# Performance work log

Measured on AMD Instinct MI355X. Metric: run time of the kernel, lower is better.

The kernel has to match this reference:

```python
import jax, jax.numpy as jnp
import numpy as np

N_HEADS = 16
D_MODEL = 1024
TOTAL = 8192
N_SEQ = 8
SEQ_LEN = TOTAL // N_SEQ


def setup_inputs() -> dict:
    key = jax.random.key(0)
    ks = jax.random.split(key, 12)
    f = jnp.float32
    d = D_MODEL
    inp = {
        "query": jax.random.normal(ks[0], (TOTAL, d), f),
        "key": jax.random.normal(ks[1], (TOTAL, d), f),
        "value": jax.random.normal(ks[2], (TOTAL, d), f),
        "seq_lengths_q": jnp.full((N_SEQ,), SEQ_LEN, jnp.int64 if jax.config.jax_enable_x64 else jnp.int32),
        "seq_lengths_kv": jnp.full((N_SEQ,), SEQ_LEN, jnp.int64 if jax.config.jax_enable_x64 else jnp.int32),
        "Wq": jax.random.normal(ks[3], (d, d), f) * 0.02,
        "bq": jnp.zeros((d,), f),
        "Wk": jax.random.normal(ks[4], (d, d), f) * 0.02,
        "bk": jnp.zeros((d,), f),
        "Wv": jax.random.normal(ks[5], (d, d), f) * 0.02,
        "bv": jnp.zeros((d,), f),
        "Wo": jax.random.normal(ks[6], (d, d), f) * 0.02,
        "bo": jnpp if False else jnp.zeros((d,), f),
    }
    return inp


def reference(query, key, value, seq_lengths_q, seq_lengths_kv, Wq, bq, Wk, bk, Wv, bv, Wo, bo):
    Tq, d = query.shape
    Tkv = key.shape[0]
    H = N_HEADS
    Dh = d // H
    B = seq_lengths_q.shape[0]
    Lq = Tq // B  # equal-length packed sequences
    Lkv = Tkv // B
    scale = 1.0 / jnp.sqrt(jnp.asarray(Dh, query.dtype))

    # torch Linear: x @ W.T + b
    Q = (query @ Wq.T + bq).reshape(H, Tq, Dh)   # NOTE: raw view, no transpose
    K = (key @ Wk.T + bk).reshape(H, Tkv, Dh)    # (replicates original's view semantics)
    V = (value @ Wv.T + bv).reshape(H, Tkv, Dh)

    # Block-diagonal mask over equal-length sequences == per-block attention.
    Qb = Q.reshape(H, B, Lq, Dh)
    Kb = K.reshape(H, B, Lkv, Dh)
    Vb = V.reshape(H, B, Lkv, Dh)

    scores = jnp.einsum("hbqd,hbkd->hbqk", Qb, Kb) * scale  # [H,B,Lq,Lkv]
    probs = jax.nn.softmax(scores, axis=-1)
    attn = jnp.einsum("hbqk,hbkd->hbqd", probs, Vb)          # [H,B,Lq,Dh]

    attn = attn.reshape(H, Tq, Dh).reshape(Tq, d)  # matches .view(total_q, d_model)
    out = attn @ Wo.T + bo
    return out
```

## Files before the change

kernel.cpp:

```cpp
#include <hip/hip_runtime.h>
#include <hip/hip_bf16.h>

#define TOTAL   8192
#define DMODEL  1024
#define NHEADS  16
#define NSEQ    8
#define DH      64

typedef float  f32x4 __attribute__((ext_vector_type(4)));
typedef short  s16x8 __attribute__((ext_vector_type(8)));
typedef unsigned short u16;
typedef u16    u16x8 __attribute__((ext_vector_type(8)));

__device__ __forceinline__ u16 f2bf_rne(float x) {
  union { float f; unsigned u; } v; v.f = x;
  unsigned r = v.u + 0x7FFFu + ((v.u >> 16) & 1u);
  return (u16)(r >> 16);
}

__device__ __forceinline__ void async_cp16(const u16* g, u16* l) {
  __builtin_amdgcn_global_load_lds(
      (const __attribute__((address_space(1))) unsigned int*)g,
      (__attribute__((address_space(3))) unsigned int*)l, 16, 0, 0);
}

__global__ __launch_bounds__(256) void cvt8(const float* __restrict__ src,
                                            u16* __restrict__ dst) {
  long i = ((long)blockIdx.x * 256 + threadIdx.x) * 8;
  float4 a = *reinterpret_cast<const float4*>(src + i);
  float4 b = *reinterpret_cast<const float4*>(src + i + 4);
  u16x8 o;
  o[0] = f2bf_rne(a.x); o[1] = f2bf_rne(a.y); o[2] = f2bf_rne(a.z); o[3] = f2bf_rne(a.w);
  o[4] = f2bf_rne(b.x); o[5] = f2bf_rne(b.y); o[6] = f2bf_rne(b.z); o[7] = f2bf_rne(b.w);
  *reinterpret_cast<u16x8*>(dst + i) = o;
}

template<bool OUT_BF16>
__global__ __launch_bounds__(256) void gemm_nt_async(const u16* __restrict__ A,
                                                     const u16* __restrict__ B,
                                                     const float* __restrict__ bias,
                                                     void* __restrict__ Cp) {
  __shared__ u16 As[128 * 32];
  __shared__ u16 Bs[128 * 32];
  const int tid  = threadIdx.x;
  const int lane = tid & 63;
  const int wv   = tid >> 6;
  const int quad = lane >> 4;
  const int m16  = lane & 15;
  const int wm   = (wv & 1) * 64;
  const int wn   = (wv >> 1) * 64;
  const long bm0 = (long)blockIdx.x * 128;
  const long bn0 = (long)blockIdx.y * 128;

  const int srow = lane >> 2;
  const int sk8  = (lane & 3) * 8;

  f32x4 acc[4][4] = {};

  const u16* Abase = A + bm0 * DMODEL;
  const u16* Bbase = B + bn0 * DMODEL;

  for (int k0 = 0; k0 < DMODEL; k0 += 32) {
    #pragma unroll
    for (int j = 0; j < 2; j++) {
      const int r   = j * 4 + wv;
      const int row = r * 16 + srow;
      async_cp16(Abase + (long)row * DMODEL + k0 + sk8, &As[r * 512]);
      async_cp16(Bbase + (long)row * DMODEL + k0 + sk8, &Bs[r * 512]);
    }
    __syncthreads();

    s16x8 af[4], bfr[4];
    #pragma unroll
    for (int i = 0; i < 4; i++)
      af[i] = *(const s16x8*)&As[(wm + i * 16 + m16) * 32 + quad * 8];
    #pragma unroll
    for (int j = 0; j < 4; j++)
      bfr[j] = *(const s16x8*)&Bs[(wn + j * 16 + m16) * 32 + quad * 8];
    #pragma unroll
    for (int i = 0; i < 4; i++)
      #pragma unroll
      for (int j = 0; j < 4; j++)
        acc[i][j] = __builtin_amdgcn_mfma_f32_16x16x32_bf16(af[i], bfr[j], acc[i][j], 0, 0, 0);
    __syncthreads();
  }

  #pragma unroll
  for (int j = 0; j < 4; j++) {
    const long col = bn0 + wn + j * 16 + m16;
    const float bj = bias[col];
    #pragma unroll
    for (int i = 0; i < 4; i++) {
      const long row0 = bm0 + wm + i * 16 + quad * 4;
      #pragma unroll
      for (int r = 0; r < 4; r++) {
        float v = acc[i][j][r] + bj;
        if constexpr (OUT_BF16)
          ((u16*)Cp)[(row0 + r) * DMODEL + col] = f2bf_rne(v);
        else
          ((float*)Cp)[(row0 + r) * DMODEL + col] = v;
      }
    }
  }
}

__global__ __launch_bounds__(256) void transpose_v(const u16* __restrict__ Vbf,
                                                   u16* __restrict__ Vt) {
  constexpr int TP = 72;
  __shared__ u16 tile[64 * TP];
  const int tid = threadIdx.x;
  const long base = (long)blockIdx.y * 65536;
  const int kt = blockIdx.x;
  {
    int k = tid >> 2, dh0 = (tid & 3) * 16;
    const u16* g = Vbf + base + (long)(kt * 64 + k) * 64 + dh0;
    u16x8 a = ((const u16x8*)g)[0];
    u16x8 b = ((const u16x8*)g)[1];
    #pragma unroll
    for (int i = 0; i < 8; i++) tile[(dh0 + i) * TP + k] = a[i];
    #pragma unroll
    for (int i = 0; i < 8; i++) tile[(dh0 + 8 + i) * TP + k] = b[i];
  }
  __syncthreads();
  {
    int dh = tid >> 2, k0 = (tid & 3) * 16;
    u16x8 a = *(const u16x8*)&tile[dh * TP + k0];
    u16x8 b = *(const u16x8*)&tile[dh * TP + k0 + 8];
    u16* g = Vt + base + (long)dh * 1024 + kt * 64 + k0;
    ((u16x8*)g)[0] = a;
    ((u16x8*)g)[1] = b;
  }
}

__global__ __launch_bounds__(256) void attn_kernel(const u16* __restrict__ Qbf,
                                                   const u16* __restrict__ Kbf,
                                                   const u16* __restrict__ Vt,
                                                   u16* __restrict__ Obf) {
  constexpr int KP = 72;
  constexpr int EP = 76;
  __shared__ u16 Ks[64 * KP];
  __shared__ u16 Vs[64 * KP];
  __shared__ u16 Es[4 * 16 * EP];
  const int tid  = threadIdx.x;
  const int lane = tid & 63;
  const int wv   = tid >> 6;
  const int quad = lane >> 4;
  const int m16  = lane & 15;
  const int qt   = blockIdx.y;
  const long base = (long)blockIdx.x * 65536;

  const int qrow = qt * 64 + wv * 16;
  s16x8 aq[2];
  #pragma unroll
  for (int s = 0; s < 2; s++)
    aq[s] = *(const s16x8*)(Qbf + base + (long)(qrow + m16) * 64 + s * 32 + quad * 8);

  f32x4 acc_o[4];
  f32x4 acc_d = {0.f, 0.f, 0.f, 0.f};
  #pragma unroll
  for (int n = 0; n < 4; n++) acc_o[n] = acc_d;

  union { u16x8 u; s16x8 s; } onesu;
  u16 ov = (m16 == 0) ? (u16)0x3F80 : (u16)0;
  #pragma unroll
  for (int i = 0; i < 8; i++) onesu.u[i] = ov;
  const s16x8 bones = onesu.s;

  const float SC = 0.125f * 1.44269504088896340736f;
  const int sr = tid >> 2;
  const int sk = (tid & 3) * 16;

  for (int nt = 0; nt < 16; nt++) {
    {
      const u16* g = Kbf + base + nt * 4096 + (long)sr * 64 + sk;
      u16x8 a = ((const u16x8*)g)[0];
      u16x8 b = ((const u16x8*)g)[1];
      *(u16x8*)&Ks[sr * KP + sk]     = a;
      *(u16x8*)&Ks[sr * KP + sk + 8] = b;
    }
    {
      const u16* g = Vt + base + (long)sr * 1024 + nt * 64 + sk;
      u16x8 a = ((const u16x8*)g)[0];
      u16x8 b = ((const u16x8*)g)[1];
      *(u16x8*)&Vs[sr * KP + sk]     = a;
      *(u16x8*)&Vs[sr * KP + sk + 8] = b;
    }
    __syncthreads();

    #pragma unroll
    for (int n = 0; n < 4; n++) {
      s16x8 bk0 = *(const s16x8*)&Ks[(n * 16 + m16) * KP + quad * 8];
      s16x8 bk1 = *(const s16x8*)&Ks[(n * 16 + m16) * KP + 32 + quad * 8];
      f32x4 s = {0.f, 0.f, 0.f, 0.f};
      s = __builtin_amdgcn_mfma_f32_16x16x32_bf16(aq[0], bk0, s, 0, 0, 0);
      s = __builtin_amdgcn_mfma_f32_16x16x32_bf16(aq[1], bk1, s, 0, 0, 0);
      #pragma unroll
      for (int r = 0; r < 4; r++) {
        float e = __builtin_amdgcn_exp2f(s[r] * SC);
        Es[(wv * 16 + quad * 4 + r) * EP + n * 16 + m16] = f2bf_rne(e);
      }
    }
    s16x8 ae0 = *(const s16x8*)&Es[(wv * 16 + m16) * EP + quad * 8];
    s16x8 ae1 = *(const s16x8*)&Es[(wv * 16 + m16) * EP + 32 + quad * 8];
    #pragma unroll
    for (int n = 0; n < 4; n++) {
      s16x8 bv0 = *(const s16x8*)&Vs[(n * 16 + m16) * KP + quad * 8];
      s16x8 bv1 = *(const s16x8*)&Vs[(n * 16 + m16) * KP + 32 + quad * 8];
      acc_o[n] = __builtin_amdgcn_mfma_f32_16x16x32_bf16(ae0, bv0, acc_o[n], 0, 0, 0);
      acc_o[n] = __builtin_amdgcn_mfma_f32_16x16x32_bf16(ae1, bv1, acc_o[n], 0, 0, 0);
    }
    acc_d = __builtin_amdgcn_mfma_f32_16x16x32_bf16(ae0, bones, acc_d, 0, 0, 0);
    acc_d = __builtin_amdgcn_mfma_f32_16x16x32_bf16(ae1, bones, acc_d, 0, 0, 0);
    __syncthreads();
  }

  #pragma unroll
  for (int r = 0; r < 4; r++) {
    float d = __shfl(acc_d[r], lane & 48);
    float rinv = 1.0f / d;
    const long orow = base + (long)(qrow + quad * 4 + r) * 64;
    #pragma unroll
    for (int n = 0; n < 4; n++)
      Obf[orow + n * 16 + m16] = f2bf_rne(acc_o[n][r] * rinv);
  }
}

extern "C" void kernel_launch(void* const* d_in, const int* in_sizes, int n_in,
                              void* d_out, int out_size, void* d_ws, size_t ws_size,
                              hipStream_t stream) {
  const float* query = (const float*)d_in[0];
  const float* key_  = (const float*)d_in[1];
  const float* value = (const float*)d_in[2];
  const float* Wq = (const float*)d_in[5];
  const float* bq = (const float*)d_in[6];
  const float* Wk = (const float*)d_in[7];
  const float* bk = (const float*)d_in[8];
  const float* Wv = (const float*)d_in[9];
  const float* bv = (const float*)d_in[10];
  const float* Wo = (const float*)d_in[11];
  const float* bo = (const float*)d_in[12];

  char* ws = (char*)d_ws;
  u16* Wbf = (u16*)(ws);
  u16* Xbf = (u16*)(ws + (8l << 20));
  u16* Qbf = (u16*)(ws + (24l << 20));
  u16* Kbf = (u16*)(ws + (40l << 20));
  u16* Vbf = (u16*)(ws + (56l << 20));
  u16* Vt  = Xbf;
  u16* Obf = Vbf;

  cvt8<<<512, 256, 0, stream>>>(Wq, Wbf + 0 * 1048576);
  cvt8<<<512, 256, 0, stream>>>(Wk, Wbf + 1 * 1048576);
  cvt8<<<512, 256, 0, stream>>>(Wv, Wbf + 2 * 1048576);
  cvt8<<<512, 256, 0, stream>>>(Wo, Wbf + 3 * 1048576);

  cvt8<<<4096, 256, 0, stream>>>(query, Xbf);
  gemm_nt_async<true><<<dim3(64, 8), 256, 0, stream>>>(Xbf, Wbf + 0 * 1048576, bq, Qbf);
  cvt8<<<4096, 256, 0, stream>>>(key_, Xbf);
  gemm_nt_async<true><<<dim3(64, 8), 256, 0, stream>>>(Xbf, Wbf + 1 * 1048576, bk, Kbf);
  cvt8<<<4096, 256, 0, stream>>>(value, Xbf);
  gemm_nt_async<true><<<dim3(64, 8), 256, 0, stream>>>(Xbf, Wbf + 2 * 1048576, bv, Vbf);

  transpose_v<<<dim3(16, 128), 256, 0, stream>>>(Vbf, Vt);

  attn_kernel<<<dim3(128, 16), 256, 0, stream>>>(Qbf, Kbf, Vt, Obf);

  gemm_nt_async<false><<<dim3(64, 8), 256, 0, stream>>>(Obf, Wbf + 3 * 1048576, bo, (float*)d_out);
}
```

Baseline: 356.0 us.

## Batch QKV projections into one launch and double query rows per attention block

Merges the four weight conversions into one launch. When the workspace is large enough, it also merges the three input conversions and the three QKV GEMMs into single batched launches using a z-grid. The attention kernel now processes 128 query rows per block (32 per wave), so each K/V tile loaded into shared memory is reused across twice as many queries, and the grid shrinks accordingly. This cuts launch overhead and per-row K/V traffic, at the cost of more registers and shared memory per block and a fallback path that depends on workspace size.

```diff
diff --git a/kernel.cpp b/kernel.cpp
--- a/kernel.cpp
+++ b/kernel.cpp
@@ -24,15 +24,103 @@
       (__attribute__((address_space(3))) unsigned int*)l, 16, 0, 0);
 }
 
-__global__ __launch_bounds__(256) void cvt8(const float* __restrict__ src,
-                                            u16* __restrict__ dst) {
-  long i = ((long)blockIdx.x * 256 + threadIdx.x) * 8;
+__device__ __forceinline__ void cvt8_one(const float* __restrict__ src,
+                                         u16* __restrict__ dst, long i) {
   float4 a = *reinterpret_cast<const float4*>(src + i);
   float4 b = *reinterpret_cast<const float4*>(src + i + 4);
   u16x8 o;
   o[0] = f2bf_rne(a.x); o[1] = f2bf_rne(a.y); o[2] = f2bf_rne(a.z); o[3] = f2bf_rne(a.w);
   o[4] = f2bf_rne(b.x); o[5] = f2bf_rne(b.y); o[6] = f2bf_rne(b.z); o[7] = f2bf_rne(b.w);
   *reinterpret_cast<u16x8*>(dst + i) = o;
+}
+
+__global__ __launch_bounds__(256) void cvt8(const float* __restrict__ src,
+                                            u16* __restrict__ dst) {
+  cvt8_one(src, dst, ((long)blockIdx.x * 256 + threadIdx.x) * 8);
+}
+
+__global__ __launch_bounds__(256) void cvt8_w4(const float* __restrict__ w0,
+                                               const float* __restrict__ w1,
+                                               const float* __restrict__ w2,
+                                               const float* __restrict__ w3,
+                                               u16* __restrict__ dst) {
+  const float* srcs[4] = {w0, w1, w2, w3};
+  cvt8_one(srcs[blockIdx.y], dst + (long)blockIdx.y * (DMODEL * (long)DMODEL),
+           ((long)blockIdx.x * 256 + threadIdx.x) * 8);
+}
+
+__global__ __launch_bounds__(256) void cvt8_x3(const float* __restrict__ x0,
+                                               const float* __restrict__ x1,
+                                               const float* __restrict__ x2,
+                                               u16* __restrict__ dst) {
+  const float* srcs[3] = {x0, x1, x2};
+  cvt8_one(srcs[blockIdx.y], dst + (long)blockIdx.y * (TOTAL * (long)DMODEL),
+           ((long)blockIdx.x * 256 + threadIdx.x) * 8);
+}
+
+template<bool OUT_BF16>
+__device__ __forceinline__ void gemm_core(const u16* __restrict__ A,
+                                          const u16* __restrict__ B,
+                                          const float* __restrict__ bias,
+                                          void* __restrict__ Cp,
+                                          long bm0, long bn0,
+                                          u16* As, u16* Bs) {
+  const int tid  = threadIdx.x;
+  const int lane = tid & 63;
+  const int wv   = tid >> 6;
+  const int quad = lane >> 4;
+  const int m16  = lane & 15;
+  const int wm   = (wv & 1) * 64;
+  const int wn   = (wv >> 1) * 64;
+  const int srow = lane >> 2;
+  const int sk8  = (lane & 3) * 8;
+
+  f32x4 acc[4][4] = {};
+  const u16* Abase = A + bm0 * DMODEL;
+  const u16* Bbase = B + bn0 * DMODEL;
+
+  for (int k0 = 0; k0 < DMODEL; k0 += 32) {
+    #pragma unroll
+    for (int j = 0; j < 2; j++) {
+      const int r   = j * 4 + wv;
+      const int row = r * 16 + srow;
+      async_cp16(Abase + (long)row * DMODEL + k0 + sk8, &As[r * 512]);
+      async_cp16(Bbase + (long)row * DMODEL + k0 + sk8, &Bs[r * 512]);
+    }
+    __syncthreads();
+
+    s16x8 af[4], bfr[4];
+    #pragma unroll
+    for (int i = 0; i < 4; i++)
+      af[i] = *(const s16x8*)&As[(wm + i * 16 + m16) * 32 + quad * 8];
+    #pragma unroll
+    for (int j = 0; j < 4; j++)
+      bfr[j] = *(const s16x8*)&Bs[(wn + j * 16 + m16) * 32 + quad * 8];
+    #pragma unroll
+    for (int i = 0; i < 4; i++)
+      #pragma unroll
+      for (int j = 0; j < 4; j++)
+        acc[i][j] = __builtin_amdgcn_mfma_f32_16x16x32_bf16(af[i], bfr[j], acc[i][j], 0, 0, 0);
+    __syncthreads();
+  }
+
+  #pragma unroll
+  for (int j = 0; j < 4; j++) {
+    const long col = bn0 + wn + j * 16 + m16;
+    const float bj = bias[col];
+    #pragma unroll
+    for (int i = 0; i < 4; i++) {
+      const long row0 = bm0 + wm + i * 16 + quad * 4;
+      #pragma unroll
+      for (int r = 0; r < 4; r++) {
+        float v = acc[i][j][r] + bj;
+        if constexpr (OUT_BF16)
+          ((u16*)Cp)[(row0 + r) * DMODEL + col] = f2bf_rne(v);
+        else
+          ((float*)Cp)[(row0 + r) * DMODEL + col] = v;
+      }
+    }
+  }
 }
 
 template<bool OUT_BF16>
@@ -42,66 +130,25 @@
                                                      void* __restrict__ Cp) {
   __shared__ u16 As[128 * 32];
   __shared__ u16 Bs[128 * 32];
-  const int tid  = threadIdx.x;
-  const int lane = tid & 63;
-  const int wv   = tid >> 6;
-  const int quad = lane >> 4;
-  const int m16  = lane & 15;
-  const int wm   = (wv & 1) * 64;
-  const int wn   = (wv >> 1) * 64;
-  const long bm0 = (long)blockIdx.x * 128;
-  const long bn0 = (long)blockIdx.y * 128;
-
-  const int srow = lane >> 2;
-  const int sk8  = (lane & 3) * 8;
-
-  f32x4 acc[4][4] = {};
-
-  const u16* Abase = A + bm0 * DMODEL;
-  const u16* Bbase = B + bn0 * DMODEL;
-
-  for (int k0 = 0; k0 < DMODEL; k0 += 32) {
-    #pragma unroll
-    for (int j = 0; j < 2; j++) {
-      const int r   = j * 4 + wv;
-      const int row = r * 16 + srow;
-      async_cp16(Abase + (long)row * DMODEL + k0 + sk8, &As[r * 512]);
-      async_cp16(Bbase + (long)row * DMODEL + k0 + sk8, &Bs[r * 512]);
-    }
-    __syncthreads();
-
-    s16x8 af[4], bfr[4];
-    #pragma unroll
-    for (int i = 0; i < 4; i++)
-      af[i] = *(const s16x8*)&As[(wm + i * 16 + m16) * 32 + quad * 8];
-    #pragma unroll
-    for (int j = 0; j < 4; j++)
-      bfr[j] = *(const s16x8*)&Bs[(wn + j * 16 + m16) * 32 + quad * 8];
-    #pragma unroll
-    for (int i = 0; i < 4; i++)
-      #pragma unroll
-      for (int j = 0; j < 4; j++)
-        acc[i][j] = __builtin_amdgcn_mfma_f32_16x16x32_bf16(af[i], bfr[j], acc[i][j], 0, 0, 0);
-    __syncthreads();
-  }
-
-  #pragma unroll
-  for (int j = 0; j < 4; j++) {
-    const long col = bn0 + wn + j * 16 + m16;
-    const float bj = bias[col];
-    #pragma unroll
-    for (int i = 0; i < 4; i++) {
-      const long row0 = bm0 + wm + i * 16 + quad * 4;
-      #pragma unroll
-      for (int r = 0; r < 4; r++) {
-        float v = acc[i][j][r] + bj;
-        if constexpr (OUT_BF16)
-          ((u16*)Cp)[(row0 + r) * DMODEL + col] = f2bf_rne(v);
-        else
-          ((float*)Cp)[(row0 + r) * DMODEL + col] = v;
-      }
-    }
-  }
+  gemm_core<OUT_BF16>(A, B, bias, Cp,
+                      (long)blockIdx.x * 128, (long)blockIdx.y * 128, As, Bs);
+}
+
+__global__ __launch_bounds__(256) void gemm_qkv(const u16* __restrict__ X3,
+                                                const u16* __restrict__ W3,
+                                                const float* __restrict__ bq,
+                                                const float* __restrict__ bk,
+                                                const float* __restrict__ bv,
+                                                u16* __restrict__ QKV) {
+  __shared__ u16 As[128 * 32];
+  __shared__ u16 Bs[128 * 32];
+  const int z = blockIdx.z;
+  const float* bias = (z == 0) ? bq : (z == 1) ? bk : bv;
+  gemm_core<true>(X3 + (long)z * (TOTAL * (long)DMODEL),
+                  W3 + (long)z * (DMODEL * (long)DMODEL),
+                  bias,
+                  QKV + (long)z * (TOTAL * (long)DMODEL),
+                  (long)blockIdx.x * 128, (long)blockIdx.y * 128, As, Bs);
 }
 
 __global__ __launch_bounds__(256) void transpose_v(const u16* __restrict__ Vbf,
@@ -137,10 +184,9 @@
                                                    const u16* __restrict__ Vt,
                                                    u16* __restrict__ Obf) {
   constexpr int KP = 72;
-  constexpr int EP = 76;
   __shared__ u16 Ks[64 * KP];
   __shared__ u16 Vs[64 * KP];
-  __shared__ u16 Es[4 * 16 * EP];
+  __shared__ u16 Es[4 * 32 * KP];
   const int tid  = threadIdx.x;
   const int lane = tid & 63;
   const int wv   = tid >> 6;
@@ -149,16 +195,16 @@
   const int qt   = blockIdx.y;
   const long base = (long)blockIdx.x * 65536;
 
-  const int qrow = qt * 64 + wv * 16;
-  s16x8 aq[2];
+  const int qrow0 = qt * 128 + wv * 32;
+  s16x8 aq[2][2];
   #pragma unroll
-  for (int s = 0; s < 2; s++)
-    aq[s] = *(const s16x8*)(Qbf + base + (long)(qrow + m16) * 64 + s * 32 + quad * 8);
-
-  f32x4 acc_o[4];
-  f32x4 acc_d = {0.f, 0.f, 0.f, 0.f};
-  #pragma unroll
-  for (int n = 0; n < 4; n++) acc_o[n] = acc_d;
+  for (int g = 0; g < 2; g++)
+    #pragma unroll
+    for (int s = 0; s < 2; s++)
+      aq[g][s] = *(const s16x8*)(Qbf + base + (long)(qrow0 + g * 16 + m16) * 64 + s * 32 + quad * 8);
+
+  f32x4 acc_o[2][4] = {};
+  f32x4 acc_d[2] = {};
 
   union { u16x8 u; s16x8 s; } onesu;
   u16 ov = (m16 == 0) ? (u16)0x3F80 : (u16)0;
@@ -191,38 +237,53 @@
     for (int n = 0; n < 4; n++) {
       s16x8 bk0 = *(const s16x8*)&Ks[(n * 16 + m16) * KP + quad * 8];
       s16x8 bk1 = *(const s16x8*)&Ks[(n * 16 + m16) * KP + 32 + quad * 8];
-      f32x4 s = {0.f, 0.f, 0.f, 0.f};
-      s = __builtin_amdgcn_mfma_f32_16x16x32_bf16(aq[0], bk0, s, 0, 0, 0);
-      s = __builtin_amdgcn_mfma_f32_16x16x32_bf16(aq[1], bk1, s, 0, 0, 0);
-      #pragma unroll
-      for (int r = 0; r < 4; r++) {
-        float e = __builtin_amdgcn_exp2f(s[r] * SC);
-        Es[(wv * 16 + quad * 4 + r) * EP + n * 16 + m16] = f2bf_rne(e);
+      #pragma unroll
+      for (int g = 0; g < 2; g++) {
+        f32x4 s = {0.f, 0.f, 0.f, 0.f};
+        s = __builtin_amdgcn_mfma_f32_16x16x32_bf16(aq[g][0], bk0, s, 0, 0, 0);
+        s = __builtin_amdgcn_mfma_f32_16x16x32_bf16(aq[g][1], bk1, s, 0, 0, 0);
+        #pragma unroll
+        for (int r = 0; r < 4; r++) {
+          float e = __builtin_amdgcn_exp2f(s[r] * SC);
+          Es[(wv * 32 + g * 16 + quad * 4 + r) * KP + n * 16 + m16] = f2bf_rne(e);
+        }
       }
     }
-    s16x8 ae0 = *(const s16x8*)&Es[(wv * 16 + m16) * EP + quad * 8];
-    s16x8 ae1 = *(const s16x8*)&Es[(wv * 16 + m16) * EP + 32 + quad * 8];
+    s16x8 ae[2][2];
+    #pragma unroll
+    for (int g = 0; g < 2; g++) {
+      ae[g][0] = *(const s16x8*)&Es[(wv * 32 + g * 16 + m16) * KP + quad * 8];
+      ae[g][1] = *(const s16x8*)&Es[(wv * 32 + g * 16 + m16) * KP + 32 + quad * 8];
+    }
     #pragma unroll
     for (int n = 0; n < 4; n++) {
       s16x8 bv0 = *(const s16x8*)&Vs[(n * 16 + m16) * KP + quad * 8];
       s16x8 bv1 = *(const s16x8*)&Vs[(n * 16 + m16) * KP + 32 + quad * 8];
-      acc_o[n] = __builtin_amdgcn_mfma_f32_16x16x32_bf16(ae0, bv0, acc_o[n], 0, 0, 0);
-      acc_o[n] = __builtin_amdgcn_mfma_f32_16x16x32_bf16(ae1, bv1, acc_o[n], 0, 0, 0);
-    }
-    acc_d = __builtin_amdgcn_mfma_f32_16x16x32_bf16(ae0, bones, acc_d, 0, 0, 0);
-    acc_d = __builtin_amdgcn_mfma_f32_16x16x32_bf16(ae1, bones, acc_d, 0, 0, 0);
+      #pragma unroll
+      for (int g = 0; g < 2; g++) {
+        acc_o[g][n] = __builtin_amdgcn_mfma_f32_16x16x32_bf16(ae[g][0], bv0, acc_o[g][n], 0, 0, 0);
+        acc_o[g][n] = __builtin_amdgcn_mfma_f32_16x16x32_bf16(ae[g][1], bv1, acc_o[g][n], 0, 0, 0);
+      }
+    }
+    #pragma unroll
+    for (int g = 0; g < 2; g++) {
+      acc_d[g] = __builtin_amdgcn_mfma_f32_16x16x32_bf16(ae[g][0], bones, acc_d[g], 0, 0, 0);
+      acc_d[g] = __builtin_amdgcn_mfma_f32_16x16x32_bf16(ae[g][1], bones, acc_d[g], 0, 0, 0);
+    }
     __syncthreads();
   }
 
   #pragma unroll
-  for (int r = 0; r < 4; r++) {
-    float d = __shfl(acc_d[r], lane & 48);
-    float rinv = 1.0f / d;
-    const long orow = base + (long)(qrow + quad * 4 + r) * 64;
-    #pragma unroll
-    for (int n = 0; n < 4; n++)
-      Obf[orow + n * 16 + m16] = f2bf_rne(acc_o[n][r] * rinv);
-  }
+  for (int g = 0; g < 2; g++)
+    #pragma unroll
+    for (int r = 0; r < 4; r++) {
+      float d = __shfl(acc_d[g][r], lane & 48);
+      float rinv = 1.0f / d;
+      const long orow = base + (long)(qrow0 + g * 16 + quad * 4 + r) * 64;
+      #pragma unroll
+      for (int n = 0; n < 4; n++)
+        Obf[orow + n * 16 + m16] = f2bf_rne(acc_o[g][n][r] * rinv);
+    }
 }
 
 extern "C" void kernel_launch(void* const* d_in, const int* in_sizes, int n_in,
@@ -241,29 +302,42 @@
   const float* bo = (const float*)d_in[12];
 
   char* ws = (char*)d_ws;
-  u16* Wbf = (u16*)(ws);
-  u16* Xbf = (u16*)(ws + (8l << 20));
-  u16* Qbf = (u16*)(ws + (24l << 20));
-  u16* Kbf = (u16*)(ws + (40l << 20));
-  u16* Vbf = (u16*)(ws + (56l << 20));
-  u16* Vt  = Xbf;
-  u16* Obf = Vbf;
-
-  cvt8<<<512, 256, 0, stream>>>(Wq, Wbf + 0 * 1048576);
-  cvt8<<<512, 256, 0, stream>>>(Wk, Wbf + 1 * 1048576);
-  cvt8<<<512, 256, 0, stream>>>(Wv, Wbf + 2 * 1048576);
-  cvt8<<<512, 256, 0, stream>>>(Wo, Wbf + 3 * 1048576);
-
-  cvt8<<<4096, 256, 0, stream>>>(query, Xbf);
-  gemm_nt_async<true><<<dim3(64, 8), 256, 0, stream>>>(Xbf, Wbf + 0 * 1048576, bq, Qbf);
-  cvt8<<<4096, 256, 0, stream>>>(key_, Xbf);
-  gemm_nt_async<true><<<dim3(64, 8), 256, 0, stream>>>(Xbf, Wbf + 1 * 1048576, bk, Kbf);
-  cvt8<<<4096, 256, 0, stream>>>(value, Xbf);
-  gemm_nt_async<true><<<dim3(64, 8), 256, 0, stream>>>(Xbf, Wbf + 2 * 1048576, bv, Vbf);
-
-  transpose_v<<<dim3(16, 128), 256, 0, stream>>>(Vbf, Vt);
-
-  attn_kernel<<<dim3(128, 16), 256, 0, stream>>>(Qbf, Kbf, Vt, Obf);
-
-  gemm_nt_async<false><<<dim3(64, 8), 256, 0, stream>>>(Obf, Wbf + 3 * 1048576, bo, (float*)d_out);
-}
+  const size_t FUSED_NEED = 104ull << 20;
+
+  if (ws_size >= FUSED_NEED) {
+    u16* Wbf = (u16*)(ws);
+    u16* QKV = (u16*)(ws + (8l << 20));
+    u16* Qbf = QKV;
+    u16* Kbf = QKV + 1 * (TOTAL * (long)DMODEL);
+    u16* Vbf = QKV + 2 * (TOTAL * (long)DMODEL);
+    u16* X3  = (u16*)(ws + (56l << 20));
+    u16* Vt  = X3;
+    u16* Obf = Vbf;
+
+    cvt8_w4<<<dim3(512, 4), 256, 0, stream>>>(Wq, Wk, Wv, Wo, Wbf);
+    cvt8_x3<<<dim3(4096, 3), 256, 0, stream>>>(query, key_, value, X3);
+    gemm_qkv<<<dim3(64, 8, 3), 256, 0, stream>>>(X3, Wbf, bq, bk, bv, QKV);
+    transpose_v<<<dim3(16, 128), 256, 0, stream>>>(Vbf, Vt);
+    attn_kernel<<<dim3(128, 8), 256, 0, stream>>>(Qbf, Kbf, Vt, Obf);
+    gemm_nt_async<false><<<dim3(64, 8), 256, 0, stream>>>(Obf, Wbf + 3 * 1048576, bo, (float*)d_out);
+  } else {
+    u16* Wbf = (u16*)(ws);
+    u16* Xbf = (u16*)(ws + (8l << 20));
+    u16* Qbf = (u16*)(ws + (24l << 20));
+    u16* Kbf = (u16*)(ws + (40l << 20));
+    u16* Vbf = (u16*)(ws + (56l << 20));
+    u16* Vt  = Xbf;
+    u16* Obf = Vbf;
+
+    cvt8_w4<<<dim3(512, 4), 256, 0, stream>>>(Wq, Wk, Wv, Wo, Wbf);
+    cvt8<<<4096, 256, 0, stream>>>(query, Xbf);
+    gemm_nt_async<true><<<dim3(64, 8), 256, 0, stream>>>(Xbf, Wbf + 0 * 1048576, bq, Qbf);
+    cvt8<<<4096, 256, 0, stream>>>(key_, Xbf);
+    gemm_nt_async<true><<<dim3(64, 8), 256, 0, stream>>>(Xbf, Wbf + 1 * 1048576, bk, Kbf);
+    cvt8<<<4096, 256, 0, stream>>>(value, Xbf);
+    gemm_nt_async<true><<<dim3(64, 8), 256, 0, stream>>>(Xbf, Wbf + 2 * 1048576, bv, Vbf);
+    transpose_v<<<dim3(16, 128), 256, 0, stream>>>(Vbf, Vt);
+    attn_kernel<<<dim3(128, 8), 256, 0, stream>>>(Qbf, Kbf, Vt, Obf);
+    gemm_nt_async<false><<<dim3(64, 8), 256, 0, stream>>>(Obf, Wbf + 3 * 1048576, bo, (float*)d_out);
+  }
+}
```

Result: faster. 326.5 us (-8.3%).
